# Kernel optimization log

Measured on AMD Instinct MI355X. Metric: run time of the kernel, lower is better.

The kernel has to match this reference:

```python
import jax, jax.numpy as jnp
import numpy as np

B, S, D, H, DH = 2, 4096, 1024, 8, 128
BLK, TOPK = 512, 4
NBLK = S // BLK
EPS = 1e-5
NEG = -1e9


def _rope_tables():
    pos = np.arange(S, dtype=np.float32)
    inv = 1.0 / (10000.0 ** (np.arange(0, DH, 2, dtype=np.float32) / DH))
    ang = pos[:, None] * inv[None, :]              # [S, DH/2]
    cos = np.concatenate([np.cos(ang), np.cos(ang)], axis=-1)  # [S, DH]
    sin = np.concatenate([np.sin(ang), np.sin(ang)], axis=-1)
    return jnp.asarray(cos), jnp.asarray(sin)


def setup_inputs() -> dict:
    key = jax.random.key(0)
    ks = jax.random.split(key, 8)
    sc = 0.02
    cos, sin = _rope_tables()
    return {
        "hidden_states": jax.random.normal(ks[0], (B, S, D), jnp.float32),
        "ln1_w": jnp.ones((D,), jnp.float32), "ln1_b": jnp.zeros((D,), jnp.float32),
        "wq": jax.random.normal(ks[1], (D, D), jnp.float32) * sc, "bq": jnp.zeros((D,), jnp.float32),
        "wk": jax.random.normal(ks[2], (D, D), jnp.float32) * sc, "bk": jnp.zeros((D,), jnp.float32),
        "wv": jax.random.normal(ks[3], (D, D), jnp.float32) * sc, "bv": jnp.zeros((D,), jnp.float32),
        "wo": jax.random.normal(ks[4], (D, D), jnp.float32) * sc, "bo": jnp.zeros((D,), jnp.float32),
        "ln2_w": jnp.ones((D,), jnp.float32), "ln2_b": jnp.zeros((D,), jnp.float32),
        "wi": jax.random.normal(ks[5], (D, 4 * D), jnp.float32) * sc, "bi": jnp.zeros((4 * D,), jnp.float32),
        "wo2": jax.random.normal(ks[6], (4 * D, D), jnp.float32) * sc, "bo2": jnp.zeros((D,), jnp.float32),
        "cos": cos, "sin": sin,
    }


def _ln(x, w, b):
    mu = x.mean(-1, keepdims=True)
    var = ((x - mu) ** 2).mean(-1, keepdims=True)
    return (x - mu) * jax.lax.rsqrt(var + EPS) * w + b


def _rotate_half(x):
    x1, x2 = jnp.split(x, 2, axis=-1)
    return jnp.concatenate([-x2, x1], axis=-1)


def _moba_attn(x, wq, bq, wk, bk, wv, bv, wo, bo, cos, sin):
    # projections -> [B, H, S, DH]
    def heads(t):
        return t.reshape(B, S, H, DH).transpose(0, 2, 1, 3)
    q = heads(x @ wq + bq)
    k = heads(x @ wk + bk)
    v = heads(x @ wv + bv)
    c = cos[None, None]; s = sin[None, None]
    q = q * c + _rotate_half(q) * s
    k = k * c + _rotate_half(k) * s
    scale = 1.0 / jnp.sqrt(jnp.asarray(DH, q.dtype))

    # block routing: mean-pooled keys per block -> gate scores [B,H,S,NBLK]
    kmean = k.reshape(B, H, NBLK, BLK, DH).mean(axis=3)
    gate = jnp.einsum("bhsd,bhnd->bhsn", q, kmean) * scale
    pos = jnp.arange(S)
    blk_start = jnp.arange(NBLK) * BLK
    visible = blk_start[None, :] <= pos[:, None]            # [S, NBLK] block has >=1 causal key
    gate = jnp.where(visible[None, None], gate, NEG)
    _, top_idx = jax.lax.top_k(gate, TOPK)                  # [B,H,S,TOPK]
    sel = jax.nn.one_hot(top_idx, NBLK, dtype=jnp.float32).sum(-2)  # [B,H,S,NBLK]
    cur = jax.nn.one_hot(pos // BLK, NBLK, dtype=jnp.float32)       # always attend own block
    sel_blocks = (sel + cur[None, None]) > 0
    sel_keys = jnp.repeat(sel_blocks, BLK, axis=-1)          # [B,H,S,S]

    scores = jnp.einsum("bhid,bhjd->bhij", q, k) * scale
    causal = pos[None, :] <= pos[:, None]
    mask = sel_keys & causal[None, None]
    scores = jnp.where(mask, scores, NEG)
    probs = jax.nn.softmax(scores, axis=-1)
    out = jnp.einsum("bhij,bhjd->bhid", probs, v)
    out = out.transpose(0, 2, 1, 3).reshape(B, S, D)
    return out @ wo + bo


def reference(hidden_states, ln1_w, ln1_b, wq, bq, wk, bk, wv, bv, wo, bo,
              ln2_w, ln2_b, wi, bi, wo2, bo2, cos, sin):
    residual = hidden_states
    x = _ln(hidden_states, ln1_w, ln1_b)
    x = residual + _moba_attn(x, wq, bq, wk, bk, wv, bv, wo, bo, cos, sin)
    residual = x
    h = _ln(x, ln2_w, ln2_b)
    h = jax.nn.gelu(h @ wi + bi, approximate=False)
    h = h @ wo2 + bo2
    return residual + h
```

## Files before the change

### kernel.cpp

```cpp
#include <hip/hip_runtime.h>
#include <cstdint>

#define S_LEN 4096
#define NHEAD 8
#define DHEAD 128
#define DMODEL 1024
#define MOBA_TOPK 4

typedef __attribute__((ext_vector_type(8))) short short8;
typedef __attribute__((ext_vector_type(4))) float f32x4;

__device__ inline float bf2f(short s) {
  return __builtin_bit_cast(float, (unsigned)((unsigned short)s) << 16);
}
__device__ inline short f2bf(float f) {
  unsigned u = __builtin_bit_cast(unsigned, f);
  unsigned r = (u + 0x7fffu + ((u >> 16) & 1u)) >> 16;
  return (short)(unsigned short)r;
}
__device__ inline float toF(float v) { return v; }
__device__ inline float toF(short v) { return bf2f(v); }

#define MFMA(a, b, c) __builtin_amdgcn_mfma_f32_16x16x32_bf16(a, b, c, 0, 0, 0)
#define GLOAD_LDS(gsrc, ldst)                                                  \
  __builtin_amdgcn_global_load_lds(                                            \
      (const __attribute__((address_space(1))) void*)(gsrc),                   \
      (__attribute__((address_space(3))) void*)(ldst), 16, 0, 0)

template <typename T>
__global__ __launch_bounds__(256) void transpose_bf16(const T* __restrict__ in,
                                                      short* __restrict__ out,
                                                      int R, int C) {
  __shared__ float tile[32][33];
  size_t bo = (size_t)blockIdx.z * R * C;
  int c0 = blockIdx.x * 32, r0 = blockIdx.y * 32;
  int tx = threadIdx.x & 31, ty = threadIdx.x >> 5;
#pragma unroll
  for (int i = 0; i < 32; i += 8)
    tile[ty + i][tx] = toF(in[bo + (size_t)(r0 + ty + i) * C + c0 + tx]);
  __syncthreads();
#pragma unroll
  for (int i = 0; i < 32; i += 8)
    out[bo + (size_t)(c0 + ty + i) * R + r0 + tx] = f2bf(tile[tx][ty + i]);
}

__global__ __launch_bounds__(256) void pack_bias(const float* __restrict__ bq,
                                                 const float* __restrict__ bk,
                                                 const float* __restrict__ bv,
                                                 float* __restrict__ dst) {
  int i = blockIdx.x * 256 + threadIdx.x;
  const float* src = (i < 1024) ? bq : (i < 2048) ? bk : bv;
  dst[i] = src[i & 1023];
}

__global__ __launch_bounds__(256) void ln_kernel(const float* __restrict__ x,
                                                 const float* __restrict__ w,
                                                 const float* __restrict__ b,
                                                 short* __restrict__ out) {
  int row = blockIdx.x * 4 + (threadIdx.x >> 6);
  int lane = threadIdx.x & 63;
  const float* xr = x + (size_t)row * DMODEL + lane * 16;
  f32x4 v[4];
  float sum = 0.f, sq = 0.f;
#pragma unroll
  for (int i = 0; i < 4; ++i) {
    v[i] = *(const f32x4*)(xr + i * 4);
#pragma unroll
    for (int j = 0; j < 4; ++j) {
      sum += v[i][j];
      sq += v[i][j] * v[i][j];
    }
  }
#pragma unroll
  for (int d = 1; d < 64; d <<= 1) {
    sum += __shfl_xor(sum, d, 64);
    sq += __shfl_xor(sq, d, 64);
  }
  float mu = sum * (1.f / DMODEL);
  float var = sq * (1.f / DMODEL) - mu * mu;
  float rstd = rsqrtf(var + 1e-5f);
  short* orow = out + (size_t)row * DMODEL;
#pragma unroll
  for (int i = 0; i < 4; ++i)
#pragma unroll
    for (int j = 0; j < 4; ++j) {
      int c = lane * 16 + i * 4 + j;
      orow[c] = f2bf((v[i][j] - mu) * rstd * w[c] + b[c]);
    }
}

template <int BN, int WM, int MODE>
__global__ __launch_bounds__(512, 2) void gemm256(const short* __restrict__ A,
                                                  const short* __restrict__ BT,
                                                  const float* __restrict__ bias,
                                                  const float* __restrict__ residF,
                                                  short* __restrict__ outB,
                                                  float* outF, int M, int N,
                                                  int K) {
  constexpr int MF = 16 / WM;
  constexpr int NWN = 8 / WM;
  constexpr int RB = BN / 64;
  __shared__ alignas(16) short As[2][16384];
  __shared__ alignas(16) short Bs[2][BN * 64];

  const int t = threadIdx.x, lane = t & 63, w = t >> 6;
  const int wm = w / NWN, wn = w % NWN;
  const int m0 = blockIdx.y * 256, n0 = blockIdx.x * BN;
  const int wmBase = wm * (256 / WM);
  const int wnBase = wn * 64;
  const int lr = lane & 15;
  const int koff0 = ((((lane >> 4) << 4)) ^ ((lane & 7) << 4)) >> 1;
  const int koff1 = ((64 + ((lane >> 4) << 4)) ^ ((lane & 7) << 4)) >> 1;

  const f32x4 fz = {0.f, 0.f, 0.f, 0.f};
  f32x4 acc[MF][4];
#pragma unroll
  for (int i = 0; i < MF; ++i)
#pragma unroll
    for (int j = 0; j < 4; ++j) acc[i][j] = fz;

  auto stageA = [&](short* dst, int k0) {
#pragma unroll
    for (int rd = 0; rd < 4; ++rd) {
      int p = (t << 4) + (rd << 13);
      int row = p >> 7;
      int ks = ((p & 127) ^ ((row & 7) << 4)) >> 1;
      GLOAD_LDS(A + (size_t)(m0 + row) * K + k0 + ks, dst + (p >> 1));
    }
  };
  auto stageB = [&](short* dst, int k0) {
#pragma unroll
    for (int rd = 0; rd < RB; ++rd) {
      int p = (t << 4) + (rd << 13);
      int row = p >> 7;
      int ks = ((p & 127) ^ ((row & 7) << 4)) >> 1;
      GLOAD_LDS(BT + (size_t)(n0 + row) * K + k0 + ks, dst + (p >> 1));
    }
  };

  const int NT = K >> 6;
  stageA(&As[0][0], 0);
  stageB(&Bs[0][0], 0);
  __syncthreads();

  for (int kt = 0; kt < NT; ++kt) {
    const int cur = kt & 1;
    if (kt + 1 < NT) {
      stageA(&As[cur ^ 1][0], (kt + 1) << 6);
      stageB(&Bs[cur ^ 1][0], (kt + 1) << 6);
    }
    __builtin_amdgcn_sched_barrier(0);
    short8 bfr[4][2];
#pragma unroll
    for (int ni = 0; ni < 4; ++ni) {
      int rb = (wnBase + ni * 16 + lr) << 6;
      bfr[ni][0] = *(const short8*)(&Bs[cur][rb + koff0]);
      bfr[ni][1] = *(const short8*)(&Bs[cur][rb + koff1]);
    }
#pragma unroll
    for (int pp = 0; pp < MF / 2; ++pp) {
      const int ra0 = (wmBase + (pp * 2) * 16 + lr) << 6;
      const int ra1 = (wmBase + (pp * 2 + 1) * 16 + lr) << 6;
      short8 a00 = *(const short8*)(&As[cur][ra0 + koff0]);
      short8 a01 = *(const short8*)(&As[cur][ra0 + koff1]);
      short8 a10 = *(const short8*)(&As[cur][ra1 + koff0]);
      short8 a11 = *(const short8*)(&As[cur][ra1 + koff1]);
      __builtin_amdgcn_sched_barrier(0);
      __builtin_amdgcn_s_setprio(1);
#pragma unroll
      for (int ni = 0; ni < 4; ++ni) {
        acc[pp * 2][ni] = MFMA(a00, bfr[ni][0], acc[pp * 2][ni]);
        acc[pp * 2][ni] = MFMA(a01, bfr[ni][1], acc[pp * 2][ni]);
        acc[pp * 2 + 1][ni] = MFMA(a10, bfr[ni][0], acc[pp * 2 + 1][ni]);
        acc[pp * 2 + 1][ni] = MFMA(a11, bfr[ni][1], acc[pp * 2 + 1][ni]);
      }
      __builtin_amdgcn_s_setprio(0);
      __builtin_amdgcn_sched_barrier(0);
    }
    __syncthreads();
  }

  const int er = lane >> 4, ec = lane & 15;
#pragma unroll
  for (int mi = 0; mi < MF; ++mi) {
#pragma unroll
    for (int ni = 0; ni < 4; ++ni) {
      int col = n0 + wnBase + ni * 16 + ec;
      float bs = bias[col];
#pragma unroll
      for (int r = 0; r < 4; ++r) {
        int row = m0 + wmBase + mi * 16 + er * 4 + r;
        float v = acc[mi][ni][r] + bs;
        size_t idx = (size_t)row * N + col;
        if (MODE == 1) {
          v += residF[idx];
          outF[idx] = v;
        } else if (MODE == 2) {
          float gl = 0.5f * v * (1.f + erff(v * 0.70710678118654752f));
          outB[idx] = f2bf(gl);
        } else if (MODE == 3) {
          v += outF[idx];
          outF[idx] = v;
        } else {
          int b = row >> 12, s = row & 4095;
          int tens = col >> 10, rem = col & 1023;
          int h = rem >> 7, dh = rem & 127;
          outB[(size_t)tens * 8388608 +
               ((size_t)((b * NHEAD + h) * S_LEN + s)) * DHEAD + dh] = f2bf(v);
        }
      }
    }
  }
}

__global__ __launch_bounds__(256) void rope_kernel(short* __restrict__ q,
                                                   short* __restrict__ k,
                                                   const float* __restrict__ cosT,
                                                   const float* __restrict__ sinT) {
  int row = blockIdx.x * 4 + (threadIdx.x >> 6);
  int lane = threadIdx.x & 63;
  int s = row & (S_LEN - 1);
  float c1 = cosT[s * DHEAD + lane], s1 = sinT[s * DHEAD + lane];
  float c2 = cosT[s * DHEAD + 64 + lane], s2 = sinT[s * DHEAD + 64 + lane];
  size_t base = (size_t)row * DHEAD;
  float a = bf2f(q[base + lane]), bb = bf2f(q[base + 64 + lane]);
  q[base + lane] = f2bf(a * c1 - bb * s1);
  q[base + 64 + lane] = f2bf(bb * c2 + a * s2);
  a = bf2f(k[base + lane]);
  bb = bf2f(k[base + 64 + lane]);
  k[base + lane] = f2bf(a * c1 - bb * s1);
  k[base + 64 + lane] = f2bf(bb * c2 + a * s2);
}

__global__ __launch_bounds__(256) void kmean_kernel(const short* __restrict__ K,
                                                    float* __restrict__ kmean) {
  int n = blockIdx.x, bh = blockIdx.y;
  int t = threadIdx.x;
  int d = t & 127, half = t >> 7;
  const short* base = K + ((size_t)bh * S_LEN + n * 512 + half * 256) * DHEAD + d;
  float s = 0.f;
  for (int i = 0; i < 256; ++i) s += bf2f(base[(size_t)i * DHEAD]);
  __shared__ float red[256];
  red[t] = s;
  __syncthreads();
  if (t < 128)
    kmean[((size_t)bh * 8 + n) * DHEAD + d] = (red[t] + red[t + 128]) * (1.f / 512.f);
}

__global__ __launch_bounds__(256) void gate_kernel(const short* __restrict__ Q,
                                                   const float* __restrict__ kmean,
                                                   unsigned* __restrict__ selmask) {
  int bh = blockIdx.x >> 4;
  int s = ((blockIdx.x & 15) << 8) + threadIdx.x;
  __shared__ float km[8 * DHEAD];
  for (int i = threadIdx.x; i < 8 * DHEAD; i += 256)
    km[i] = kmean[(size_t)bh * 8 * DHEAD + i];
  __syncthreads();
  const short* qrow = Q + ((size_t)bh * S_LEN + s) * DHEAD;
  float g[8] = {0, 0, 0, 0, 0, 0, 0, 0};
  for (int c = 0; c < 16; ++c) {
    short8 qv = *(const short8*)(qrow + c * 8);
    float qf[8];
#pragma unroll
    for (int j = 0; j < 8; ++j) qf[j] = bf2f(qv[j]);
#pragma unroll
    for (int n = 0; n < 8; ++n) {
      float a = 0.f;
#pragma unroll
      for (int j = 0; j < 8; ++j) a += qf[j] * km[n * DHEAD + c * 8 + j];
      g[n] += a;
    }
  }
  int own = s >> 9;
  int nvis = own + 1;
  int kcnt = nvis < MOBA_TOPK ? nvis : MOBA_TOPK;
  unsigned used = 0;
  for (int it = 0; it < kcnt; ++it) {
    float best = -1e38f;
    int bi = 0;
    for (int n = 0; n < nvis; ++n)
      if (!((used >> n) & 1) && g[n] > best) {
        best = g[n];
        bi = n;
      }
    used |= 1u << bi;
  }
  selmask[(size_t)bh * S_LEN + s] = used | (1u << own);
}

__global__ __launch_bounds__(512, 2) void attn_kernel(
    const short* __restrict__ Q, const short* __restrict__ K,
    const short* __restrict__ VT, const unsigned* __restrict__ selmask,
    short* __restrict__ out) {
  const int t = threadIdx.x, lane = t & 63, w = t >> 6;
  const int er = lane >> 4, ec = lane & 15;

  __shared__ alignas(16) short kbuf[2][8192];
  __shared__ alignas(16) short vbuf[8192];
  __shared__ alignas(16) short plds[8][1152];
  __shared__ unsigned selS[128];
  __shared__ unsigned umS[2];
  __shared__ int kbsS[66];

  for (int pass = 0; pass < 2; ++pass) {
    const int u = pass ? (511 - (int)blockIdx.x) : (int)blockIdx.x;
    const int qt = u & 31, bh = u >> 5;
    const int b = bh >> 3, h = bh & 7;
    const int q0t = qt << 7;

    if (t < 128) selS[t] = selmask[(size_t)bh * S_LEN + q0t + t];
    __syncthreads();
    if (w < 2) {
      unsigned v = selS[w * 64 + lane];
#pragma unroll
      for (int d = 1; d < 64; d <<= 1) v |= __shfl_xor(v, d, 64);
      if (lane == 0) umS[w] = v;
    }
    __syncthreads();
    if (t == 0) {
      unsigned um = umS[0] | umS[1];
      int qmax = q0t + 127;
      int maxb = qmax >> 9;
      int n = 0;
      for (int kb = 0; kb <= maxb; ++kb)
        if ((um >> kb) & 1) {
          int subs = (kb == maxb) ? (((qmax - (kb << 9)) >> 6) + 1) : 8;
          for (int s2 = 0; s2 < subs; ++s2) kbsS[n++] = (kb << 9) + (s2 << 6);
        }
      kbsS[64] = n;
    }
    __syncthreads();
    const int nIter = kbsS[64];

    const size_t sbh = (size_t)bh * S_LEN * DHEAD;
    const short* Kg = K + sbh;
    const short* Vg = VT + (size_t)bh * DHEAD * S_LEN;

    auto kstage = [&](short* dst, int key0) {
#pragma unroll
      for (int rnd = 0; rnd < 2; ++rnd) {
        int p = (t + rnd * 512) << 4;
        int key = p >> 8;
        int lin = p ^ ((key & 7) << 4);
        GLOAD_LDS(Kg + (size_t)(key0 + key) * DHEAD + ((lin & 255) >> 1),
                  dst + (p >> 1));
      }
    };
    auto vstage = [&](int key0) {
#pragma unroll
      for (int rnd = 0; rnd < 2; ++rnd) {
        int p = (t + rnd * 512) << 4;
        int dh = p >> 7;
        int lin = p ^ ((dh & 7) << 4);
        GLOAD_LDS(Vg + (size_t)dh * S_LEN + key0 + ((lin & 127) >> 1),
                  vbuf + (p >> 1));
      }
    };

    const int q0w = q0t + w * 16;
    short8 qf[4];
#pragma unroll
    for (int ks = 0; ks < 4; ++ks)
      qf[ks] = *(const short8*)(Q + sbh + (size_t)(q0w + ec) * DHEAD + ks * 32 + er * 8);

    unsigned selw[4];
    int qq[4];
#pragma unroll
    for (int r = 0; r < 4; ++r) {
      selw[r] = selS[w * 16 + er * 4 + r];
      qq[r] = q0w + er * 4 + r;
    }

    const f32x4 fz = {0.f, 0.f, 0.f, 0.f};
    f32x4 oacc[8];
#pragma unroll
    for (int n = 0; n < 8; ++n) oacc[n] = fz;
    float mrow[4] = {-1e30f, -1e30f, -1e30f, -1e30f};
    float lrow[4] = {0.f, 0.f, 0.f, 0.f};
    const float scale = 0.088388347648318447f;
    short* pl = &plds[w][0];

    kstage(&kbuf[0][0], kbsS[0]);
    int cur = 0;
    for (int it = 0; it < nIter; ++it) {
      const int key0 = kbsS[it];
      const int kb = key0 >> 9;
      const int key0n = kbsS[(it + 1 < nIter) ? it + 1 : it];
      vstage(key0);
      kstage(&kbuf[cur ^ 1][0], key0n);
      asm volatile("s_waitcnt vmcnt(4)" ::: "memory");
      __builtin_amdgcn_sched_barrier(0);
      __builtin_amdgcn_s_barrier();
      __builtin_amdgcn_sched_barrier(0);

      const short* kl = &kbuf[cur][0];
      f32x4 sc[4];
#pragma unroll
      for (int kh = 0; kh < 4; ++kh) {
        short8 kf[4];
#pragma unroll
        for (int ks = 0; ks < 4; ++ks) {
          int slot = ((ks << 2) + er) ^ (ec & 7);
          kf[ks] = *(const short8*)(kl + (((kh << 4) + ec) << 7) + (slot << 3));
        }
        f32x4 a = fz;
#pragma unroll
        for (int ks = 0; ks < 4; ++ks) a = MFMA(qf[ks], kf[ks], a);
        sc[kh] = a;
      }

      float corr[4];
#pragma unroll
      for (int r = 0; r < 4; ++r) {
        const bool sb = (selw[r] >> kb) & 1;
        const int kqoff = qq[r] - key0 - ec;
        const bool ok0 = sb && (0 <= kqoff);
        const bool ok1 = sb && (16 <= kqoff);
        const bool ok2 = sb && (32 <= kqoff);
        const bool ok3 = sb && (48 <= kqoff);
        float s0 = sc[0][r] * scale, s1 = sc[1][r] * scale;
        float s2 = sc[2][r] * scale, s3 = sc[3][r] * scale;
        float m0 = ok0 ? s0 : -1e30f, m1 = ok1 ? s1 : -1e30f;
        float m2 = ok2 ? s2 : -1e30f, m3 = ok3 ? s3 : -1e30f;
        float mx = fmaxf(fmaxf(m0, m1), fmaxf(m2, m3));
#pragma unroll
        for (int d = 1; d < 16; d <<= 1) mx = fmaxf(mx, __shfl_xor(mx, d, 64));
        const float mnew = fmaxf(mrow[r], mx);
        const float c = __expf(mrow[r] - mnew);
        const float e0 = ok0 ? __expf(s0 - mnew) : 0.f;
        const float e1 = ok1 ? __expf(s1 - mnew) : 0.f;
        const float e2 = ok2 ? __expf(s2 - mnew) : 0.f;
        const float e3 = ok3 ? __expf(s3 - mnew) : 0.f;
        float rs = e0 + e1 + e2 + e3;
#pragma unroll
        for (int d = 1; d < 16; d <<= 1) rs += __shfl_xor(rs, d, 64);
        lrow[r] = lrow[r] * c + rs;
        mrow[r] = mnew;
        corr[r] = c;
        const int prow = (er * 4 + r) * 72;
        pl[prow + ec] = f2bf(e0);
        pl[prow + 16 + ec] = f2bf(e1);
        pl[prow + 32 + ec] = f2bf(e2);
        pl[prow + 48 + ec] = f2bf(e3);
      }
      asm volatile("s_waitcnt lgkmcnt(0)" ::: "memory");
      __builtin_amdgcn_sched_barrier(0);
      const short8 pa0 = *(const short8*)(pl + ec * 72 + er * 8);
      const short8 pa1 = *(const short8*)(pl + ec * 72 + 32 + er * 8);

#pragma unroll
      for (int n = 0; n < 8; ++n)
#pragma unroll
        for (int r = 0; r < 4; ++r) oacc[n][r] *= corr[r];

      asm volatile("s_waitcnt vmcnt(2)" ::: "memory");
      __builtin_amdgcn_sched_barrier(0);
      __builtin_amdgcn_s_barrier();
      __builtin_amdgcn_sched_barrier(0);

#pragma unroll
      for (int kc = 0; kc < 2; ++kc) {
        const short8 pa = kc ? pa1 : pa0;
#pragma unroll
        for (int n = 0; n < 8; ++n) {
          int slot = ((kc << 2) + er) ^ (ec & 7);
          short8 vf = *(const short8*)(vbuf + (((n << 4) + ec) << 6) + (slot << 3));
          oacc[n] = MFMA(pa, vf, oacc[n]);
        }
      }
      __builtin_amdgcn_sched_barrier(0);
      __builtin_amdgcn_s_barrier();
      __builtin_amdgcn_sched_barrier(0);
      cur ^= 1;
    }

#pragma unroll
    for (int n = 0; n < 8; ++n) {
#pragma unroll
      for (int r = 0; r < 4; ++r) {
        float v = oacc[n][r] / lrow[r];
        out[((size_t)(b * S_LEN + qq[r])) * DMODEL + h * DHEAD + n * 16 + ec] = f2bf(v);
      }
    }
    asm volatile("s_waitcnt vmcnt(0)" ::: "memory");
    __syncthreads();
  }
}

extern "C" void kernel_launch(void* const* d_in, const int* in_sizes, int n_in,
                              void* d_out, int out_size, void* d_ws,
                              size_t ws_size, hipStream_t stream) {
  (void)in_sizes; (void)n_in; (void)out_size; (void)ws_size;
  const float* hidden = (const float*)d_in[0];
  const float* ln1w = (const float*)d_in[1];
  const float* ln1b = (const float*)d_in[2];
  const float* wq = (const float*)d_in[3];
  const float* bq = (const float*)d_in[4];
  const float* wk = (const float*)d_in[5];
  const float* bk = (const float*)d_in[6];
  const float* wv = (const float*)d_in[7];
  const float* bv = (const float*)d_in[8];
  const float* wo = (const float*)d_in[9];
  const float* bo = (const float*)d_in[10];
  const float* ln2w = (const float*)d_in[11];
  const float* ln2b = (const float*)d_in[12];
  const float* wi = (const float*)d_in[13];
  const float* bi = (const float*)d_in[14];
  const float* wo2 = (const float*)d_in[15];
  const float* bo2 = (const float*)d_in[16];
  const float* cosT = (const float*)d_in[17];
  const float* sinT = (const float*)d_in[18];
  float* outF = (float*)d_out;

  char* base = (char*)d_ws;
  size_t off = 0;
  auto alloc = [&](size_t bytes) {
    char* p = base + off;
    off = (off + bytes + 255) & ~(size_t)255;
    return p;
  };
  short* wqkvT = (short*)alloc((size_t)3072 * 1024 * 2);
  short* woT = (short*)alloc((size_t)1024 * 1024 * 2);
  short* wiT = (short*)alloc((size_t)4096 * 1024 * 2);
  short* wo2T = (short*)alloc((size_t)1024 * 4096 * 2);
  float* biasC = (float*)alloc((size_t)3072 * 4);
  float* kmeanB = (float*)alloc((size_t)16 * 8 * 128 * 4);
  unsigned* selm = (unsigned*)alloc((size_t)16 * 4096 * 4);
  short* xattn = (short*)alloc((size_t)8192 * 1024 * 2);
  short* h2 = (short*)alloc((size_t)8192 * 1024 * 2);
  size_t phase = off;
  short* xln = (short*)alloc((size_t)8192 * 1024 * 2);
  short* qb = (short*)alloc((size_t)16 * 4096 * 128 * 2);
  short* kb = (short*)alloc((size_t)16 * 4096 * 128 * 2);
  short* vb = (short*)alloc((size_t)16 * 4096 * 128 * 2);
  short* vT = (short*)alloc((size_t)16 * 128 * 4096 * 2);
  short* g = (short*)(base + phase);

  dim3 T256(256);
  dim3 T512(512);
  transpose_bf16<float><<<dim3(32, 32, 1), T256, 0, stream>>>(wq, wqkvT, 1024, 1024);
  transpose_bf16<float><<<dim3(32, 32, 1), T256, 0, stream>>>(wk, wqkvT + 1048576, 1024, 1024);
  transpose_bf16<float><<<dim3(32, 32, 1), T256, 0, stream>>>(wv, wqkvT + 2097152, 1024, 1024);
  transpose_bf16<float><<<dim3(32, 32, 1), T256, 0, stream>>>(wo, woT, 1024, 1024);
  transpose_bf16<float><<<dim3(128, 32, 1), T256, 0, stream>>>(wi, wiT, 1024, 4096);
  transpose_bf16<float><<<dim3(32, 128, 1), T256, 0, stream>>>(wo2, wo2T, 4096, 1024);
  pack_bias<<<12, T256, 0, stream>>>(bq, bk, bv, biasC);

  ln_kernel<<<2048, T256, 0, stream>>>(hidden, ln1w, ln1b, xln);

  gemm256<256, 2, 4><<<dim3(12, 32), T512, 0, stream>>>(xln, wqkvT, biasC, nullptr, qb, nullptr, 8192, 3072, 1024);

  rope_kernel<<<16384, T256, 0, stream>>>(qb, kb, cosT, sinT);
  transpose_bf16<short><<<dim3(4, 128, 16), T256, 0, stream>>>(vb, vT, 4096, 128);

  kmean_kernel<<<dim3(8, 16), T256, 0, stream>>>(kb, kmeanB);
  gate_kernel<<<256, T256, 0, stream>>>(qb, kmeanB, selm);

  attn_kernel<<<dim3(256), T512, 0, stream>>>(qb, kb, vT, selm, xattn);

  gemm256<128, 4, 1><<<dim3(8, 32), T512, 0, stream>>>(xattn, woT, bo, hidden, nullptr, outF, 8192, 1024, 1024);
  ln_kernel<<<2048, T256, 0, stream>>>(outF, ln2w, ln2b, h2);
  gemm256<256, 2, 2><<<dim3(16, 32), T512, 0, stream>>>(h2, wiT, bi, nullptr, g, nullptr, 8192, 4096, 1024);
  gemm256<128, 4, 3><<<dim3(8, 32), T512, 0, stream>>>(g, wo2T, bo2, nullptr, nullptr, outF, 8192, 1024, 4096);
}
```

Before: 726.1 us.

## Transpose QK MFMA for per-lane row softmax with lazy rescale and exp2

Swaps the MFMA operand order so each lane holds one query row's scores, turning the per-row 16-lane max/sum reductions into two cross-group shuffles. It adds a lazy max update that rescales the output accumulators only when the running max grows by a threshold, folds the softmax scale into exp2, and packs the bf16 conversion with v_cvt_pk_bf16_f32. Launch bounds go from 2 to 4 waves per SIMD, which tightens the register budget and may cause spills. The lazy rescale relies on a bounded growth margin before the exponentials could overflow.

```diff
diff --git a/kernel.cpp b/kernel.cpp
--- a/kernel.cpp
+++ b/kernel.cpp
@@ -288,12 +288,13 @@
   selmask[(size_t)bh * S_LEN + s] = used | (1u << own);
 }
 
-__global__ __launch_bounds__(512, 2) void attn_kernel(
+__global__ __launch_bounds__(512, 4) void attn_kernel(
     const short* __restrict__ Q, const short* __restrict__ K,
     const short* __restrict__ VT, const unsigned* __restrict__ selmask,
     short* __restrict__ out) {
   const int t = threadIdx.x, lane = t & 63, w = t >> 6;
   const int er = lane >> 4, ec = lane & 15;
+  const int er4 = er << 2;
 
   __shared__ alignas(16) short kbuf[2][8192];
   __shared__ alignas(16) short vbuf[8192];
@@ -301,6 +302,8 @@
   __shared__ unsigned selS[128];
   __shared__ unsigned umS[2];
   __shared__ int kbsS[66];
+
+  const float C = 0.12751742946f;
 
   for (int pass = 0; pass < 2; ++pass) {
     const int u = pass ? (511 - (int)blockIdx.x) : (int)blockIdx.x;
@@ -363,21 +366,14 @@
     for (int ks = 0; ks < 4; ++ks)
       qf[ks] = *(const short8*)(Q + sbh + (size_t)(q0w + ec) * DHEAD + ks * 32 + er * 8);
 
-    unsigned selw[4];
-    int qq[4];
-#pragma unroll
-    for (int r = 0; r < 4; ++r) {
-      selw[r] = selS[w * 16 + er * 4 + r];
-      qq[r] = q0w + er * 4 + r;
-    }
+    const unsigned selq = selS[w * 16 + ec];
+    const int qmine = q0w + ec;
 
     const f32x4 fz = {0.f, 0.f, 0.f, 0.f};
     f32x4 oacc[8];
 #pragma unroll
     for (int n = 0; n < 8; ++n) oacc[n] = fz;
-    float mrow[4] = {-1e30f, -1e30f, -1e30f, -1e30f};
-    float lrow[4] = {0.f, 0.f, 0.f, 0.f};
-    const float scale = 0.088388347648318447f;
+    float m = -1e30f, lrow = 0.f;
     short* pl = &plds[w][0];
 
     kstage(&kbuf[0][0], kbsS[0]);
@@ -394,7 +390,7 @@
       __builtin_amdgcn_sched_barrier(0);
 
       const short* kl = &kbuf[cur][0];
-      f32x4 sc[4];
+      float s[16];
 #pragma unroll
       for (int kh = 0; kh < 4; ++kh) {
         short8 kf[4];
@@ -405,53 +401,72 @@
         }
         f32x4 a = fz;
 #pragma unroll
-        for (int ks = 0; ks < 4; ++ks) a = MFMA(qf[ks], kf[ks], a);
-        sc[kh] = a;
-      }
-
-      float corr[4];
-#pragma unroll
-      for (int r = 0; r < 4; ++r) {
-        const bool sb = (selw[r] >> kb) & 1;
-        const int kqoff = qq[r] - key0 - ec;
-        const bool ok0 = sb && (0 <= kqoff);
-        const bool ok1 = sb && (16 <= kqoff);
-        const bool ok2 = sb && (32 <= kqoff);
-        const bool ok3 = sb && (48 <= kqoff);
-        float s0 = sc[0][r] * scale, s1 = sc[1][r] * scale;
-        float s2 = sc[2][r] * scale, s3 = sc[3][r] * scale;
-        float m0 = ok0 ? s0 : -1e30f, m1 = ok1 ? s1 : -1e30f;
-        float m2 = ok2 ? s2 : -1e30f, m3 = ok3 ? s3 : -1e30f;
-        float mx = fmaxf(fmaxf(m0, m1), fmaxf(m2, m3));
-#pragma unroll
-        for (int d = 1; d < 16; d <<= 1) mx = fmaxf(mx, __shfl_xor(mx, d, 64));
-        const float mnew = fmaxf(mrow[r], mx);
-        const float c = __expf(mrow[r] - mnew);
-        const float e0 = ok0 ? __expf(s0 - mnew) : 0.f;
-        const float e1 = ok1 ? __expf(s1 - mnew) : 0.f;
-        const float e2 = ok2 ? __expf(s2 - mnew) : 0.f;
-        const float e3 = ok3 ? __expf(s3 - mnew) : 0.f;
-        float rs = e0 + e1 + e2 + e3;
-#pragma unroll
-        for (int d = 1; d < 16; d <<= 1) rs += __shfl_xor(rs, d, 64);
-        lrow[r] = lrow[r] * c + rs;
-        mrow[r] = mnew;
-        corr[r] = c;
-        const int prow = (er * 4 + r) * 72;
-        pl[prow + ec] = f2bf(e0);
-        pl[prow + 16 + ec] = f2bf(e1);
-        pl[prow + 32 + ec] = f2bf(e2);
-        pl[prow + 48 + ec] = f2bf(e3);
+        for (int ks = 0; ks < 4; ++ks) a = MFMA(kf[ks], qf[ks], a);
+#pragma unroll
+        for (int r = 0; r < 4; ++r) s[kh * 4 + r] = a[r];
+      }
+
+      int kqoff = qmine - key0 - er4;
+      if (!((selq >> kb) & 1)) kqoff = -1;
+      float mx = -1e30f;
+#pragma unroll
+      for (int kh = 0; kh < 4; ++kh)
+#pragma unroll
+        for (int r = 0; r < 4; ++r)
+          mx = fmaxf(mx, ((kh * 16 + r) <= kqoff) ? s[kh * 4 + r] : -1e30f);
+      mx = fmaxf(mx, __shfl_xor(mx, 16, 64));
+      mx = fmaxf(mx, __shfl_xor(mx, 32, 64));
+
+      if (__any(mx > m + 62.0f)) {
+        float mnew = fmaxf(m, mx);
+        float corr = __builtin_amdgcn_exp2f((m - mnew) * C);
+        m = mnew;
+        lrow *= corr;
+        float c0 = __shfl(corr, er4 + 0, 16);
+        float c1 = __shfl(corr, er4 + 1, 16);
+        float c2 = __shfl(corr, er4 + 2, 16);
+        float c3 = __shfl(corr, er4 + 3, 16);
+#pragma unroll
+        for (int n = 0; n < 8; ++n) {
+          oacc[n][0] *= c0;
+          oacc[n][1] *= c1;
+          oacc[n][2] *= c2;
+          oacc[n][3] *= c3;
+        }
+      }
+
+      const float mc = m * C;
+      float e[16];
+      float rs = 0.f;
+#pragma unroll
+      for (int kh = 0; kh < 4; ++kh)
+#pragma unroll
+        for (int r = 0; r < 4; ++r) {
+          int i = kh * 4 + r;
+          float ex = __builtin_amdgcn_exp2f(fmaf(s[i], C, -mc));
+          ex = ((kh * 16 + r) <= kqoff) ? ex : 0.f;
+          e[i] = ex;
+          rs += ex;
+        }
+      rs += __shfl_xor(rs, 16, 64);
+      rs += __shfl_xor(rs, 32, 64);
+      lrow += rs;
+
+      short* pb = pl + ec * 72 + er4;
+#pragma unroll
+      for (int kh = 0; kh < 4; ++kh) {
+        unsigned u0, u1;
+        asm("v_cvt_pk_bf16_f32 %0, %1, %2"
+            : "=v"(u0) : "v"(e[kh * 4 + 0]), "v"(e[kh * 4 + 1]));
+        asm("v_cvt_pk_bf16_f32 %0, %1, %2"
+            : "=v"(u1) : "v"(e[kh * 4 + 2]), "v"(e[kh * 4 + 3]));
+        *(unsigned*)(pb + kh * 16) = u0;
+        *(unsigned*)(pb + kh * 16 + 2) = u1;
       }
       asm volatile("s_waitcnt lgkmcnt(0)" ::: "memory");
       __builtin_amdgcn_sched_barrier(0);
       const short8 pa0 = *(const short8*)(pl + ec * 72 + er * 8);
       const short8 pa1 = *(const short8*)(pl + ec * 72 + 32 + er * 8);
-
-#pragma unroll
-      for (int n = 0; n < 8; ++n)
-#pragma unroll
-        for (int r = 0; r < 4; ++r) oacc[n][r] *= corr[r];
 
       asm volatile("s_waitcnt vmcnt(2)" ::: "memory");
       __builtin_amdgcn_sched_barrier(0);
@@ -474,12 +489,15 @@
       cur ^= 1;
     }
 
+    float rl[4];
+#pragma unroll
+    for (int r = 0; r < 4; ++r) rl[r] = 1.0f / __shfl(lrow, er4 + r, 16);
 #pragma unroll
     for (int n = 0; n < 8; ++n) {
 #pragma unroll
       for (int r = 0; r < 4; ++r) {
-        float v = oacc[n][r] / lrow[r];
-        out[((size_t)(b * S_LEN + qq[r])) * DMODEL + h * DHEAD + n * 16 + ec] = f2bf(v);
+        float v = oacc[n][r] * rl[r];
+        out[((size_t)(b * S_LEN + q0w + er4 + r)) * DMODEL + h * DHEAD + n * 16 + ec] = f2bf(v);
       }
     }
     asm volatile("s_waitcnt vmcnt(0)" ::: "memory");
```

Result: faster. 675.0 us (-7.0%).
